# Optimization experiments

Measured on AMD Instinct MI355X. Metric: run time of the kernel, lower is better.

The kernel has to match this reference:

```python
import jax, jax.numpy as jnp
import numpy as np

KERNEL_SIZE = 4
SCALE = 0.5


def setup_inputs() -> dict:
    key = jax.random.key(0)
    k1, k2, k3 = jax.random.split(key, 3)
    M, K, N = 16384, 1024, 4096
    x = jax.random.normal(k1, (M, K), dtype=jnp.float32)
    weight = jax.random.normal(k2, (N, K), dtype=jnp.float32)
    bias = jax.random.normal(k3, (N,), dtype=jnp.float32)
    return {"x": x, "weight": weight, "bias": bias}


def reference(x, weight, bias):
    # y = x @ W^T + b : (M, N)
    y = jnp.einsum('mk,nk->mn', x, weight) + bias[None, :]
    M, N = y.shape
    valid_n = (N // KERNEL_SIZE) * KERNEL_SIZE
    # MaxPool1d(kernel_size, stride=kernel_size): (M, N//k, k) -> max over window
    pooled = jnp.max(y[:, :valid_n].reshape(M, valid_n // KERNEL_SIZE, KERNEL_SIZE), axis=-1)
    # sum over pooled features, then scale -> (M,)
    return jnp.sum(pooled, axis=-1) * SCALE
```

## Files before the change

### kernel.cpp

```cpp
#include <hip/hip_runtime.h>
#include <stdint.h>

#define M_DIM 16384
#define K_DIM 1024
#define N_DIM 4096
#define BM 128
#define BN 128
#define LDSP 40

#define TILE_ELEMS (128 * K_DIM)
#define SLAB_ELEMS (128 * 32)
#define CPAD 516

typedef __bf16 bf16;
typedef __attribute__((ext_vector_type(8))) __bf16 bf16x8;
typedef __attribute__((ext_vector_type(4))) float f32x4;

__device__ __forceinline__ uint32_t pack2_bf16(float a, float b) {
    uint32_t ua = __float_as_uint(a);
    uint32_t ub = __float_as_uint(b);
    ua += 0x7fffu + ((ua >> 16) & 1u);
    ub += 0x7fffu + ((ub >> 16) & 1u);
    return (ua >> 16) | (ub & 0xffff0000u);
}

__global__ __launch_bounds__(256) void convert_pack_kernel(
    const float* __restrict__ x, const float* __restrict__ w,
    bf16* __restrict__ xp, bf16* __restrict__ wp, float* __restrict__ out)
{
    int g = blockIdx.x;
    const int t = threadIdx.x;
    if (g < (M_DIM / 256)) out[g * 256 + t] = 0.f;

    const float* src;
    bf16* dst;
    if (g < (M_DIM / 16)) {
        src = x + (size_t)g * 16 * K_DIM;  dst = xp;
    } else {
        g -= M_DIM / 16;
        src = w + (size_t)g * 16 * K_DIM;  dst = wp;
    }
    const int tile = g >> 3;
    const int rb   = g & 7;

    __shared__ uint32_t ls[16 * CPAD];

    #pragma unroll
    for (int i = 0; i < 16; ++i) {
        float4 v = ((const float4*)src)[i * 256 + t];
        uint2 d;
        d.x = pack2_bf16(v.x, v.y);
        d.y = pack2_bf16(v.z, v.w);
        *(uint2*)&ls[i * CPAD + t * 2] = d;
    }
    __syncthreads();

    const int wv = t >> 6, l = t & 63;
    const int lrow = l & 15, q = l >> 4;
    uint4* dst4 = (uint4*)(dst + (size_t)tile * TILE_ELEMS);
    #pragma unroll
    for (int it = 0; it < 8; ++it) {
        const int s = wv + it * 4;
        uint4 v = *(const uint4*)&ls[lrow * CPAD + s * 16 + q * 4];
        dst4[(s * 8 + rb) * 64 + l] = v;
    }
}

__device__ __forceinline__ void load_set(const bf16* base, uint32_t off, bf16x8* f) {
    #pragma unroll
    for (int i = 0; i < 4; ++i) f[i] = *(const bf16x8*)(base + off + i * 512);
}

__device__ __forceinline__ void do_mfma(const bf16x8* af, const bf16x8* bf,
                                        f32x4 acc[4][4]) {
    #pragma unroll
    for (int i = 0; i < 4; ++i)
        #pragma unroll
        for (int j = 0; j < 4; ++j)
            acc[i][j] = __builtin_amdgcn_mfma_f32_16x16x32_bf16(af[i], bf[j], acc[i][j], 0, 0, 0);
}

__global__ __launch_bounds__(256, 2) void gemm_pool_direct_kernel(
    const bf16* __restrict__ xp, const bf16* __restrict__ wp,
    const float* __restrict__ bias, float* __restrict__ out)
{
    const int b     = blockIdx.x;
    const int xcd   = b & 7;
    const int o     = (b >> 3) & 7;
    const int bx    = (b >> 6) & 31;
    const int phase = b >> 11;
    const int by    = phase * 64 + xcd * 8 + o;

    const int lane = threadIdx.x & 63;
    const int wave = threadIdx.x >> 6;
    const int wm = wave >> 1;
    const int wn = wave & 1;
    const int lr = lane & 15;
    const int quad = lane >> 4;

    const bf16* Ab = xp + (size_t)by * TILE_ELEMS;
    const bf16* Bb = wp + (size_t)bx * TILE_ELEMS;
    const uint32_t aoff = (wm * 4) * 512 + lane * 8;
    const uint32_t boff = (wn * 4) * 512 + lane * 8;

    f32x4 acc[4][4] = {};
    bf16x8 Af[3][4];
    bf16x8 Bf[5][4];

    load_set(Bb, boff + 0 * SLAB_ELEMS, Bf[0]);
    load_set(Bb, boff + 1 * SLAB_ELEMS, Bf[1]);
    load_set(Bb, boff + 2 * SLAB_ELEMS, Bf[2]);
    load_set(Bb, boff + 3 * SLAB_ELEMS, Bf[3]);
    load_set(Ab, aoff + 0 * SLAB_ELEMS, Af[0]);
    load_set(Ab, aoff + 1 * SLAB_ELEMS, Af[1]);

    #pragma unroll
    for (int s = 0; s < 32; ++s) {
        if (s + 4 < 32) load_set(Bb, boff + (s + 4) * SLAB_ELEMS, Bf[(s + 4) % 5]);
        if (s + 2 < 32) load_set(Ab, aoff + (s + 2) * SLAB_ELEMS, Af[(s + 2) % 3]);
        do_mfma(Af[s % 3], Bf[s % 5], acc);
    }

    float bv[4];
    #pragma unroll
    for (int j = 0; j < 4; ++j)
        bv[j] = bias[bx * BN + wn * 64 + j * 16 + lr];

    #pragma unroll
    for (int i = 0; i < 4; ++i) {
        float rs[4] = {0.f, 0.f, 0.f, 0.f};
        #pragma unroll
        for (int j = 0; j < 4; ++j) {
            #pragma unroll
            for (int r = 0; r < 4; ++r) {
                float t = acc[i][j][r] + bv[j];
                t = fmaxf(t, __shfl_xor(t, 1, 64));
                t = fmaxf(t, __shfl_xor(t, 2, 64));
                rs[r] += t;
            }
        }
        #pragma unroll
        for (int r = 0; r < 4; ++r) {
            rs[r] += __shfl_xor(rs[r], 4, 64);
            rs[r] += __shfl_xor(rs[r], 8, 64);
        }
        if (lr == 0) {
            const int row = by * BM + wm * 64 + i * 16 + quad * 4;
            #pragma unroll
            for (int r = 0; r < 4; ++r)
                atomicAdd(&out[row + r], rs[r] * 0.5f);
        }
    }
}

__global__ __launch_bounds__(256) void fused_linear_pool_kernel(
    const float* __restrict__ x, const float* __restrict__ wt,
    const float* __restrict__ bias, float* __restrict__ out)
{
    __shared__ uint32_t sA[BM * LDSP / 2];
    __shared__ uint32_t sB[BN * LDSP / 2];

    const int tid = threadIdx.x;
    const int bx = blockIdx.x;
    const int by = blockIdx.y;

    const float* Abase = x  + (size_t)by * BM * K_DIM;
    const float* Bbase = wt + (size_t)bx * BN * K_DIM;

    const int lane = tid & 63;
    const int wave = tid >> 6;
    const int wm = wave >> 1;
    const int wn = wave & 1;
    const int lr = lane & 15;
    const int quad = lane >> 4;

    const int srow  = tid >> 2;
    const int scol  = (tid & 3) * 8;
    const int swidx = (tid & 3) * 4;

    f32x4 acc[4][4] = {};

    for (int kt = 0; kt < K_DIM; kt += 32) {
        #pragma unroll
        for (int p = 0; p < 2; ++p) {
            const int r = srow + p * 64;
            const float4* ga = (const float4*)(Abase + (size_t)r * K_DIM + kt + scol);
            const float4* gb = (const float4*)(Bbase + (size_t)r * K_DIM + kt + scol);
            float4 a0 = ga[0], a1 = ga[1], b0 = gb[0], b1 = gb[1];
            uint4 wa;
            wa.x = pack2_bf16(a0.x, a0.y); wa.y = pack2_bf16(a0.z, a0.w);
            wa.z = pack2_bf16(a1.x, a1.y); wa.w = pack2_bf16(a1.z, a1.w);
            *(uint4*)&sA[r * (LDSP / 2) + swidx] = wa;
            uint4 wbv;
            wbv.x = pack2_bf16(b0.x, b0.y); wbv.y = pack2_bf16(b0.z, b0.w);
            wbv.z = pack2_bf16(b1.x, b1.y); wbv.w = pack2_bf16(b1.z, b1.w);
            *(uint4*)&sB[r * (LDSP / 2) + swidx] = wbv;
        }
        __syncthreads();

        bf16x8 af[4], bfr[4];
        #pragma unroll
        for (int i = 0; i < 4; ++i)
            af[i] = *(const bf16x8*)((const bf16*)sA + (wm * 64 + i * 16 + lr) * LDSP + quad * 8);
        #pragma unroll
        for (int j = 0; j < 4; ++j)
            bfr[j] = *(const bf16x8*)((const bf16*)sB + (wn * 64 + j * 16 + lr) * LDSP + quad * 8);

        #pragma unroll
        for (int i = 0; i < 4; ++i)
            #pragma unroll
            for (int j = 0; j < 4; ++j)
                acc[i][j] = __builtin_amdgcn_mfma_f32_16x16x32_bf16(af[i], bfr[j], acc[i][j], 0, 0, 0);
        __syncthreads();
    }

    float bv[4];
    #pragma unroll
    for (int j = 0; j < 4; ++j)
        bv[j] = bias[bx * BN + wn * 64 + j * 16 + lr];

    #pragma unroll
    for (int i = 0; i < 4; ++i) {
        float rsum[4] = {0.f, 0.f, 0.f, 0.f};
        #pragma unroll
        for (int j = 0; j < 4; ++j) {
            #pragma unroll
            for (int r = 0; r < 4; ++r) {
                float t = acc[i][j][r] + bv[j];
                t = fmaxf(t, __shfl_xor(t, 1, 64));
                t = fmaxf(t, __shfl_xor(t, 2, 64));
                t += __shfl_xor(t, 4, 64);
                t += __shfl_xor(t, 8, 64);
                rsum[r] += t;
            }
        }
        if (lr == 0) {
            const int row = by * BM + wm * 64 + i * 16 + quad * 4;
            #pragma unroll
            for (int r = 0; r < 4; ++r)
                atomicAdd(&out[row + r], rsum[r] * 0.5f);
        }
    }
}

extern "C" void kernel_launch(void* const* d_in, const int* in_sizes, int n_in,
                              void* d_out, int out_size, void* d_ws, size_t ws_size,
                              hipStream_t stream) {
    const float* x  = (const float*)d_in[0];
    const float* wt = (const float*)d_in[1];
    const float* bs = (const float*)d_in[2];
    float* out = (float*)d_out;

    const size_t xe = (size_t)M_DIM * K_DIM;
    const size_t we = (size_t)N_DIM * K_DIM;
    const size_t need = (xe + we) * sizeof(bf16);

    if (ws_size >= need) {
        bf16* xp = (bf16*)d_ws;
        bf16* wp = xp + xe;
        const int nconv = (M_DIM / 16) + (N_DIM / 16);
        convert_pack_kernel<<<nconv, 256, 0, stream>>>(x, wt, xp, wp, out);
        gemm_pool_direct_kernel<<<(M_DIM / BM) * (N_DIM / BN), 256, 0, stream>>>(xp, wp, bs, out);
    } else {
        hipMemsetAsync(out, 0, (size_t)out_size * sizeof(float), stream);
        dim3 grid(N_DIM / BN, M_DIM / BM);
        fused_linear_pool_kernel<<<grid, 256, 0, stream>>>(x, wt, bs, out);
    }
}
```

Before: 263.2 us.

## Replace register-direct GEMM with 256x256 LDS double-buffered 8-wave pipelined kernel

The fused GEMM+pool kernel now uses 256x256 block tiles with 8 waves and stages the pre-packed bf16 operands into LDS through global_load_lds, double-buffering across K chunks. Barriers, explicit vmcnt waits and s_setprio around the MFMA groups interleave the LDS fragment reads, the async global loads and the matrix math. The larger tile is meant to raise operand reuse and cut global traffic compared with each wave loading its fragments straight from global memory. In exchange it uses 128KB of LDS per block and 128 accumulator registers per lane, which limits occupancy and depends on getting the hand-written synchronisation exactly right.

Measured after the change: 246.9 us. 6.2% less time.

```diff
diff --git a/kernel.cpp b/kernel.cpp
--- a/kernel.cpp
+++ b/kernel.cpp
@@ -11,6 +11,11 @@
 #define TILE_ELEMS (128 * K_DIM)
 #define SLAB_ELEMS (128 * 32)
 #define CPAD 516
+
+#define GBM 256
+#define GBN 256
+#define CHUNK 4096
+#define BUFE  (8 * CHUNK)
 
 typedef __bf16 bf16;
 typedef __attribute__((ext_vector_type(8))) __bf16 bf16x8;
@@ -66,77 +71,134 @@
     }
 }
 
-__device__ __forceinline__ void load_set(const bf16* base, uint32_t off, bf16x8* f) {
-    #pragma unroll
-    for (int i = 0; i < 4; ++i) f[i] = *(const bf16x8*)(base + off + i * 512);
-}
-
-__device__ __forceinline__ void do_mfma(const bf16x8* af, const bf16x8* bf,
-                                        f32x4 acc[4][4]) {
-    #pragma unroll
-    for (int i = 0; i < 4; ++i)
-        #pragma unroll
-        for (int j = 0; j < 4; ++j)
-            acc[i][j] = __builtin_amdgcn_mfma_f32_16x16x32_bf16(af[i], bf[j], acc[i][j], 0, 0, 0);
-}
-
-__global__ __launch_bounds__(256, 2) void gemm_pool_direct_kernel(
+
+#define BARRIER() do { asm volatile("" ::: "memory"); \
+                       __builtin_amdgcn_s_barrier();  \
+                       asm volatile("" ::: "memory"); } while (0)
+#define VMCNT4() asm volatile("s_waitcnt vmcnt(4)" ::: "memory")
+#define VMCNT0() asm volatile("s_waitcnt vmcnt(0)" ::: "memory")
+
+#define STAGE16(ldsOff, gsrc) \
+    __builtin_amdgcn_global_load_lds( \
+        (const __attribute__((address_space(1))) unsigned int*)(gsrc), \
+        (__attribute__((address_space(3))) unsigned int*)&sm[(ldsOff) + w * 512], \
+        16, 0, 0)
+
+#define LDA4(sH, IB) do { \
+    Af[0] = *(const bf16x8*)&sm[pO + (sH) * 8192 + aBase + ((IB) + 0) * 512]; \
+    Af[1] = *(const bf16x8*)&sm[pO + (sH) * 8192 + aBase + ((IB) + 1) * 512]; \
+    Af[2] = *(const bf16x8*)&sm[pO + (sH) * 8192 + aBase + ((IB) + 2) * 512]; \
+    Af[3] = *(const bf16x8*)&sm[pO + (sH) * 8192 + aBase + ((IB) + 3) * 512]; \
+} while (0)
+
+#define LDB4(sH) do { \
+    Bf[0] = *(const bf16x8*)&sm[pO + (sH) * 8192 + bBase + 0 * 512]; \
+    Bf[1] = *(const bf16x8*)&sm[pO + (sH) * 8192 + bBase + 1 * 512]; \
+    Bf[2] = *(const bf16x8*)&sm[pO + (sH) * 8192 + bBase + 2 * 512]; \
+    Bf[3] = *(const bf16x8*)&sm[pO + (sH) * 8192 + bBase + 3 * 512]; \
+} while (0)
+
+#define MFMA16(IB) do { \
+    __builtin_amdgcn_s_setprio(1); \
+    _Pragma("unroll") \
+    for (int ii = 0; ii < 4; ++ii) \
+        _Pragma("unroll") \
+        for (int jj = 0; jj < 4; ++jj) \
+            acc[(IB) + ii][jj] = __builtin_amdgcn_mfma_f32_16x16x32_bf16( \
+                Af[ii], Bf[jj], acc[(IB) + ii][jj], 0, 0, 0); \
+    __builtin_amdgcn_s_setprio(0); \
+} while (0)
+
+#define TILE_BODY(T, P, STG) do { \
+    const int pO  = (P) * BUFE; \
+    const int pnO = ((P) ^ 1) * BUFE; \
+     \
+    LDA4(0, 0); LDB4(0); \
+    if (STG) { STAGE16(pnO + 0 * CHUNK, Ag + 0 * TILE_ELEMS + (size_t)(2 * (T) + 2) * CHUNK + toff); \
+               STAGE16(pnO + 1 * CHUNK, Ag + 1 * TILE_ELEMS + (size_t)(2 * (T) + 2) * CHUNK + toff); } \
+    BARRIER(); MFMA16(0); BARRIER(); \
+     \
+    LDA4(0, 4); \
+    if (STG) { STAGE16(pnO + 4 * CHUNK, Bg + 0 * TILE_ELEMS + (size_t)(2 * (T) + 2) * CHUNK + toff); \
+               STAGE16(pnO + 5 * CHUNK, Bg + 1 * TILE_ELEMS + (size_t)(2 * (T) + 2) * CHUNK + toff); } \
+    BARRIER(); MFMA16(4); \
+    if (STG) { VMCNT4(); } else { VMCNT0(); }    \
+    BARRIER(); \
+     \
+    LDA4(1, 0); LDB4(1); \
+    if (STG) { STAGE16(pnO + 2 * CHUNK, Ag + 0 * TILE_ELEMS + (size_t)(2 * (T) + 3) * CHUNK + toff); \
+               STAGE16(pnO + 3 * CHUNK, Ag + 1 * TILE_ELEMS + (size_t)(2 * (T) + 3) * CHUNK + toff); } \
+    BARRIER(); MFMA16(0); BARRIER(); \
+     \
+    LDA4(1, 4); \
+    if (STG) { STAGE16(pnO + 6 * CHUNK, Bg + 0 * TILE_ELEMS + (size_t)(2 * (T) + 3) * CHUNK + toff); \
+               STAGE16(pnO + 7 * CHUNK, Bg + 1 * TILE_ELEMS + (size_t)(2 * (T) + 3) * CHUNK + toff); } \
+    BARRIER(); MFMA16(4); \
+    if (STG) { VMCNT4(); }                        \
+    BARRIER(); \
+} while (0)
+
+__global__ __launch_bounds__(512, 2) void gemm_pool_8phase_kernel(
     const bf16* __restrict__ xp, const bf16* __restrict__ wp,
     const float* __restrict__ bias, float* __restrict__ out)
 {
-    const int b     = blockIdx.x;
-    const int xcd   = b & 7;
-    const int o     = (b >> 3) & 7;
-    const int bx    = (b >> 6) & 31;
-    const int phase = b >> 11;
-    const int by    = phase * 64 + xcd * 8 + o;
-
-    const int lane = threadIdx.x & 63;
-    const int wave = threadIdx.x >> 6;
-    const int wm = wave >> 1;
-    const int wn = wave & 1;
-    const int lr = lane & 15;
+    __shared__ bf16 sm[2 * BUFE];
+
+    const int b  = blockIdx.x;
+    const int bx = b & (N_DIM / GBN - 1);
+    const int by = b >> 4;
+
+    const int tid  = threadIdx.x;
+    const int lane = tid & 63;
+    const int w    = tid >> 6;
+    const int wm   = w >> 2;
+    const int wn   = w & 3;
+    const int lr   = lane & 15;
     const int quad = lane >> 4;
-
-    const bf16* Ab = xp + (size_t)by * TILE_ELEMS;
-    const bf16* Bb = wp + (size_t)bx * TILE_ELEMS;
-    const uint32_t aoff = (wm * 4) * 512 + lane * 8;
-    const uint32_t boff = (wn * 4) * 512 + lane * 8;
-
-    f32x4 acc[4][4] = {};
-    bf16x8 Af[3][4];
-    bf16x8 Bf[5][4];
-
-    load_set(Bb, boff + 0 * SLAB_ELEMS, Bf[0]);
-    load_set(Bb, boff + 1 * SLAB_ELEMS, Bf[1]);
-    load_set(Bb, boff + 2 * SLAB_ELEMS, Bf[2]);
-    load_set(Bb, boff + 3 * SLAB_ELEMS, Bf[3]);
-    load_set(Ab, aoff + 0 * SLAB_ELEMS, Af[0]);
-    load_set(Ab, aoff + 1 * SLAB_ELEMS, Af[1]);
-
-    #pragma unroll
-    for (int s = 0; s < 32; ++s) {
-        if (s + 4 < 32) load_set(Bb, boff + (s + 4) * SLAB_ELEMS, Bf[(s + 4) % 5]);
-        if (s + 2 < 32) load_set(Ab, aoff + (s + 2) * SLAB_ELEMS, Af[(s + 2) % 3]);
-        do_mfma(Af[s % 3], Bf[s % 5], acc);
-    }
+    const int toff = tid * 8;
+
+    const bf16* __restrict__ Ag = xp + (size_t)(2 * by) * TILE_ELEMS;
+    const bf16* __restrict__ Bg = wp + (size_t)(2 * bx) * TILE_ELEMS;
+
+    const int aBase = wm * CHUNK + lane * 8;
+    const int bBase = 4 * CHUNK + (wn >> 1) * CHUNK + (wn & 1) * 2048 + lane * 8;
+
+    f32x4 acc[8][4] = {};
+    bf16x8 Af[4], Bf[4];
+
+    STAGE16(0 * CHUNK, Ag + 0 * TILE_ELEMS + toff);
+    STAGE16(1 * CHUNK, Ag + 1 * TILE_ELEMS + toff);
+    STAGE16(4 * CHUNK, Bg + 0 * TILE_ELEMS + toff);
+    STAGE16(5 * CHUNK, Bg + 1 * TILE_ELEMS + toff);
+    STAGE16(2 * CHUNK, Ag + 0 * TILE_ELEMS + CHUNK + toff);
+    STAGE16(3 * CHUNK, Ag + 1 * TILE_ELEMS + CHUNK + toff);
+    STAGE16(6 * CHUNK, Bg + 0 * TILE_ELEMS + CHUNK + toff);
+    STAGE16(7 * CHUNK, Bg + 1 * TILE_ELEMS + CHUNK + toff);
+    VMCNT4(); BARRIER();
+
+    #pragma unroll
+    for (int t = 0; t < 15; ++t) {
+        const int p = t & 1;
+        TILE_BODY(t, p, 1);
+    }
+    TILE_BODY(15, 1, 0);
 
     float bv[4];
     #pragma unroll
     for (int j = 0; j < 4; ++j)
-        bv[j] = bias[bx * BN + wn * 64 + j * 16 + lr];
-
-    #pragma unroll
-    for (int i = 0; i < 4; ++i) {
+        bv[j] = bias[bx * GBN + wn * 64 + j * 16 + lr];
+
+    #pragma unroll
+    for (int i = 0; i < 8; ++i) {
         float rs[4] = {0.f, 0.f, 0.f, 0.f};
         #pragma unroll
         for (int j = 0; j < 4; ++j) {
             #pragma unroll
             for (int r = 0; r < 4; ++r) {
-                float t = acc[i][j][r] + bv[j];
-                t = fmaxf(t, __shfl_xor(t, 1, 64));
-                t = fmaxf(t, __shfl_xor(t, 2, 64));
-                rs[r] += t;
+                float v = acc[i][j][r] + bv[j];
+                v = fmaxf(v, __shfl_xor(v, 1, 64));
+                v = fmaxf(v, __shfl_xor(v, 2, 64));
+                rs[r] += v;
             }
         }
         #pragma unroll
@@ -145,7 +207,7 @@
             rs[r] += __shfl_xor(rs[r], 8, 64);
         }
         if (lr == 0) {
-            const int row = by * BM + wm * 64 + i * 16 + quad * 4;
+            const int row = by * GBM + wm * 128 + i * 16 + quad * 4;
             #pragma unroll
             for (int r = 0; r < 4; ++r)
                 atomicAdd(&out[row + r], rs[r] * 0.5f);
@@ -260,7 +322,7 @@
         bf16* wp = xp + xe;
         const int nconv = (M_DIM / 16) + (N_DIM / 16);
         convert_pack_kernel<<<nconv, 256, 0, stream>>>(x, wt, xp, wp, out);
-        gemm_pool_direct_kernel<<<(M_DIM / BM) * (N_DIM / BN), 256, 0, stream>>>(xp, wp, bs, out);
+        gemm_pool_8phase_kernel<<<(M_DIM / GBM) * (N_DIM / GBN), 512, 0, stream>>>(xp, wp, bs, out);
     } else {
         hipMemsetAsync(out, 0, (size_t)out_size * sizeof(float), stream);
         dim3 grid(N_DIM / BN, M_DIM / BM);
```
